# Optimization experiments

Measured on AMD Instinct MI355X. Metric: run time of the kernel, lower is better.

The kernel has to match this reference:

```python
import jax, jax.numpy as jnp
import numpy as np

IH, IW = 48, 48           # img_size
C = 256                   # inp == oup
NH, HD = 8, 32            # num_heads, head_dims; inner_dim = 256
HID = 4 * C               # MLP hidden
N = IH * IW               # window size (seq len) = 2304
SCALE = (C // NH) ** -0.5 # (inp_dims // num_heads) ** -0.5
EPS = 1e-5


def _relative_position_index():
    coords = np.stack(np.meshgrid(np.arange(IH), np.arange(IW), indexing='ij'))
    cf = coords.reshape(2, -1)
    rel = (cf[:, :, None] - cf[:, None, :]).transpose(1, 2, 0)
    rel[:, :, 0] += IH - 1
    rel[:, :, 1] += IW - 1
    rel[:, :, 0] *= 2 * IW - 1
    return jnp.asarray(rel.sum(-1).astype(np.int32))  # [N, N]


def setup_inputs() -> dict:
    key = jax.random.key(0)
    ks = jax.random.split(key, 12)
    s = 0.02
    return {
        'x': jax.random.normal(ks[0], (1, IH, IW, C), jnp.float32),
        'gamma1': jnp.ones((C,), jnp.float32),
        'beta1': jnp.zeros((C,), jnp.float32),
        'w_qkv': jax.random.normal(ks[1], (C, 3 * NH * HD), jnp.float32) * s,
        'w_proj': jax.random.normal(ks[2], (NH * HD, C), jnp.float32) * s,
        'b_proj': jnp.zeros((C,), jnp.float32),
        'bias_table': jax.random.normal(ks[3], ((2 * IH - 1) * (2 * IW - 1), NH), jnp.float32) * s,
        'gamma2': jnp.ones((C,), jnp.float32),
        'beta2': jnp.zeros((C,), jnp.float32),
        'w_fc1': jax.random.normal(ks[4], (C, HID), jnp.float32) * s,
        'b_fc1': jnp.zeros((HID,), jnp.float32),
        'w_fc2': jax.random.normal(ks[5], (HID, C), jnp.float32) * s,
        'b_fc2': jnp.zeros((C,), jnp.float32),
        'rel_idx': _relative_position_index(),
    }


def _layernorm(x, g, b):
    mu = jnp.mean(x, axis=-1, keepdims=True)
    var = jnp.mean(jnp.square(x - mu), axis=-1, keepdims=True)
    return (x - mu) * jax.lax.rsqrt(var + EPS) * g + b


def reference(x, gamma1, beta1, w_qkv, w_proj, b_proj, bias_table,
              gamma2, beta2, w_fc1, b_fc1, w_fc2, b_fc2, rel_idx):
    shortcut = x                                   # [1, IH, IW, C]
    t = x.reshape(1, N, C)
    t = _layernorm(t, gamma1, beta1)

    # qkv: [1, N, 3*NH*HD] -> q, k, v each [1, NH, N, HD]
    qkv = (t @ w_qkv).reshape(1, N, 3, NH, HD).transpose(2, 0, 3, 1, 4)
    q, k, v = qkv[0], qkv[1], qkv[2]
    q = q * SCALE

    attn = jnp.einsum('bhnd,bhmd->bhnm', q, k)     # [1, NH, N, N]
    # relative position bias: gather table rows by index -> [NH, N, N]
    bias = bias_table[rel_idx.reshape(-1)].reshape(N, N, NH).transpose(2, 0, 1)
    attn = jax.nn.softmax(attn + bias[None], axis=-1)

    o = jnp.einsum('bhnm,bhmd->bhnd', attn, v)     # [1, NH, N, HD]
    o = o.transpose(0, 2, 1, 3).reshape(1, N, NH * HD)
    o = o @ w_proj + b_proj                        # [1, N, C]

    x = shortcut + o.reshape(1, IH, IW, C)
    shortcut = x

    t = _layernorm(x.reshape(1, N, C), gamma2, beta2)
    t = jax.nn.gelu(t @ w_fc1 + b_fc1, approximate=False) @ w_fc2 + b_fc2
    return shortcut + t.reshape(1, IH, IW, C)
```

## Files before the change

### kernel.cpp

```cpp
#include <hip/hip_runtime.h>
#include <hip/hip_bf16.h>
#include <math.h>

#define IH 48
#define IW 48
#define NN 2304
#define CC 256
#define NH 8
#define HD 32
#define HID 1024
#define NBIAS 9025
#define SCALE 0.17677669529663687f
#define LOG2E 1.4426950408889634f
#define LN_EPS 1e-5f

typedef __attribute__((ext_vector_type(8))) short bf16x8;
typedef __attribute__((ext_vector_type(4))) float f32x4;

__device__ __forceinline__ short f2b(float f) {
    __hip_bfloat16 h = __float2bfloat16(f);
    short s; __builtin_memcpy(&s, &h, 2); return s;
}
__device__ __forceinline__ float b2f(short s) {
    __hip_bfloat16 h; __builtin_memcpy(&h, &s, 2); return __bfloat162float(h);
}
__device__ __forceinline__ float fast_exp2(float x) {
#if __has_builtin(__builtin_amdgcn_exp2f)
    return __builtin_amdgcn_exp2f(x);
#else
    return exp2f(x);
#endif
}

__global__ void prep_kernel(const float* __restrict__ x, const float* __restrict__ g,
                            const float* __restrict__ b, short* __restrict__ t1,
                            const float* __restrict__ bt, short* __restrict__ o_bias,
                            const float* __restrict__ w_qkv, const float* __restrict__ w_proj,
                            const float* __restrict__ w_fc1, const float* __restrict__ w_fc2,
                            short* __restrict__ o_qkv, short* __restrict__ o_proj,
                            short* __restrict__ o_fc1, short* __restrict__ o_fc2)
{
    __shared__ float tsh[32][33];
    __shared__ float red[8];
    const int bid = blockIdx.x, tid = threadIdx.x;
    if (bid < NN) {
        float v = x[bid * CC + tid];
        float s = v, s2 = v * v;
        #pragma unroll
        for (int off = 32; off > 0; off >>= 1) {
            s  += __shfl_xor(s, off);
            s2 += __shfl_xor(s2, off);
        }
        const int wid = tid >> 6;
        if ((tid & 63) == 0) { red[wid * 2] = s; red[wid * 2 + 1] = s2; }
        __syncthreads();
        float tot  = red[0] + red[2] + red[4] + red[6];
        float tot2 = red[1] + red[3] + red[5] + red[7];
        float mu   = tot * (1.0f / CC);
        float var  = tot2 * (1.0f / CC) - mu * mu;
        float rstd = rsqrtf(var + LN_EPS);
        t1[bid * CC + tid] = f2b((v - mu) * rstd * g[tid] + b[tid]);
        return;
    }
    if (bid < NN + 768) {
        int bb = bid - NN;
        const float* src; short* dst; int K, Nn, kt, nt;
        if (bb < 192)      { src = w_qkv;  dst = o_qkv;  K = 256;  Nn = 768;  kt = bb / 24; nt = bb % 24; }
        else if (bb < 256) { bb -= 192; src = w_proj; dst = o_proj; K = 256;  Nn = 256;  kt = bb / 8;  nt = bb % 8; }
        else if (bb < 512) { bb -= 256; src = w_fc1;  dst = o_fc1;  K = 256;  Nn = 1024; kt = bb / 32; nt = bb % 32; }
        else               { bb -= 512; src = w_fc2;  dst = o_fc2;  K = 1024; Nn = 256;  kt = bb / 8;  nt = bb % 8; }
        const int r = tid >> 5, c = tid & 31;
        const int k0 = kt * 32, n0 = nt * 32;
        #pragma unroll
        for (int i = 0; i < 4; ++i)
            tsh[r + i * 8][c] = src[(k0 + r + i * 8) * Nn + n0 + c];
        __syncthreads();
        #pragma unroll
        for (int i = 0; i < 4; ++i)
            dst[(n0 + r + i * 8) * K + k0 + c] = f2b(tsh[c][r + i * 8]);
        return;
    }
    const int stride = (gridDim.x - NN - 768) * 256;
    for (int i = (bid - NN - 768) * 256 + tid; i < NBIAS * NH; i += stride) {
        int idx = i >> 3, h = i & 7;
        o_bias[h * NBIAS + idx] = f2b(bt[i] * LOG2E);
    }
}

#define GSTRIDE 72
template<int KLEN, int KSTR, int TM>
__device__ __forceinline__ void mfma_gemm_core(const short* __restrict__ A,
                                               const short* __restrict__ BT,
                                               int m0, int n0, int kb, f32x4 acc[4],
                                               short* lds)
{
    short* As = lds;
    short* Bs = lds + TM * GSTRIDE;
    const int tid  = threadIdx.x;
    const int w    = tid >> 6, lane = tid & 63;
    const int quad = lane >> 4, l15 = lane & 15;
    const int sr = tid >> 2;
    const int sc = (tid & 3) * 16;
    #pragma unroll
    for (int c = 0; c < 4; ++c) acc[c] = (f32x4){0.f, 0.f, 0.f, 0.f};

    const short* Ap = &A [(m0 + sr) * KSTR + kb + sc];
    const short* Bp = &BT[(n0 + sr) * KSTR + kb + sc];
    bf16x8 ra0 = *(const bf16x8*)Ap,       ra1 = *(const bf16x8*)(Ap + 8);
    bf16x8 rb0 = *(const bf16x8*)Bp,       rb1 = *(const bf16x8*)(Bp + 8);
    bf16x8 rc0, rc1;
    const short* Bp2 = Bp;
    if constexpr (TM == 32) {
        Bp2 = &BT[(n0 + sr + 32) * KSTR + kb + sc];
        rc0 = *(const bf16x8*)Bp2;  rc1 = *(const bf16x8*)(Bp2 + 8);
    }

    for (int k0 = 0; k0 < KLEN; k0 += 64) {
        __syncthreads();
        *(bf16x8*)&As[sr * GSTRIDE + sc]     = ra0;
        *(bf16x8*)&As[sr * GSTRIDE + sc + 8] = ra1;
        *(bf16x8*)&Bs[sr * GSTRIDE + sc]     = rb0;
        *(bf16x8*)&Bs[sr * GSTRIDE + sc + 8] = rb1;
        if constexpr (TM == 32) {
            *(bf16x8*)&Bs[(sr + 32) * GSTRIDE + sc]     = rc0;
            *(bf16x8*)&Bs[(sr + 32) * GSTRIDE + sc + 8] = rc1;
        }
        if (k0 + 64 < KLEN) {
            ra0 = *(const bf16x8*)(Ap + k0 + 64);
            ra1 = *(const bf16x8*)(Ap + k0 + 72);
            rb0 = *(const bf16x8*)(Bp + k0 + 64);
            rb1 = *(const bf16x8*)(Bp + k0 + 72);
            if constexpr (TM == 32) {
                rc0 = *(const bf16x8*)(Bp2 + k0 + 64);
                rc1 = *(const bf16x8*)(Bp2 + k0 + 72);
            }
        }
        __syncthreads();
        #pragma unroll
        for (int s = 0; s < 2; ++s) {
            bf16x8 a = *(const bf16x8*)&As[(w * 16 + l15) * GSTRIDE + s * 32 + quad * 8];
            #pragma unroll
            for (int c = 0; c < 4; ++c) {
                bf16x8 b = *(const bf16x8*)&Bs[(c * 16 + l15) * GSTRIDE + s * 32 + quad * 8];
                acc[c] = __builtin_amdgcn_mfma_f32_16x16x32_bf16(a, b, acc[c], 0, 0, 0);
            }
        }
    }
}

__global__ void qkv_kernel(const short* __restrict__ t1, const short* __restrict__ wT,
                           short* __restrict__ qb, short* __restrict__ kb,
                           short* __restrict__ vT)
{
    __shared__ short lds[2 * 64 * GSTRIDE];
    f32x4 acc[4];
    const int m0 = blockIdx.y * 64, n0 = blockIdx.x * 64;
    mfma_gemm_core<256, 256, 64>(t1, wT, m0, n0, 0, acc, lds);
    const int lane = threadIdx.x & 63, w = threadIdx.x >> 6;
    const int quad = lane >> 4, l15 = lane & 15;
    #pragma unroll
    for (int c = 0; c < 4; ++c) {
        int col = n0 + c * 16 + l15;
        int three = col >> 8, rem = col & 255;
        int h = rem >> 5, d = rem & 31;
        #pragma unroll
        for (int r = 0; r < 4; ++r) {
            int row = m0 + w * 16 + quad * 4 + r;
            float v = acc[c][r];
            if (three == 0)      qb[(h * NN + row) * HD + d] = f2b(v * (SCALE * LOG2E));
            else if (three == 1) kb[(h * NN + row) * HD + d] = f2b(v);
            else                 vT[(h * HD + d) * NN + row] = f2b(v);
        }
    }
}

#define PSTRIDE 40
__global__ __launch_bounds__(256) void attn_kernel(
        const short* __restrict__ qb, const short* __restrict__ kb,
        const short* __restrict__ vT, const short* __restrict__ biasT,
        short* __restrict__ o)
{
    __shared__ float Ored[4][16][33];
    __shared__ float lred[4][16];
    __shared__ short sbuf[4][16 * PSTRIDE];
    __shared__ short bwin[48][64];
    const int w = threadIdx.x >> 6, lane = threadIdx.x & 63;
    const int quad = lane >> 4, l15 = lane & 15;
    const int h = blockIdx.x / 144, q0 = (blockIdx.x % 144) * 16;
    const int t0 = w * 576;
    short* sb = &sbuf[w][0];
    const short* bt = &biasT[h * NBIAS];

    const int qi = q0 / IW, qj0 = q0 % IW;

    for (int idx = threadIdx.x; idx < 48 * 63; idx += 256) {
        int kr = idx / 63, cc = idx - kr * 63;
        bwin[kr][cc] = bt[(qi - kr + 47) * 95 + qj0 + cc];
    }

    bf16x8 qf = *(const bf16x8*)&qb[(h * NN + q0 + l15) * HD + quad * 8];

    f32x4 O0 = (f32x4){0.f,0.f,0.f,0.f}, O1 = (f32x4){0.f,0.f,0.f,0.f};
    float lp[4] = {0.f, 0.f, 0.f, 0.f};
    const f32x4 zero = (f32x4){0.f,0.f,0.f,0.f};

    __syncthreads();

    for (int c = 0; c < 18; ++c) {
        const int t = t0 + c * 32;
        bf16x8 k0f = *(const bf16x8*)&kb[(h * NN + t      + l15) * HD + quad * 8];
        bf16x8 k1f = *(const bf16x8*)&kb[(h * NN + t + 16 + l15) * HD + quad * 8];
        f32x4 s0 = __builtin_amdgcn_mfma_f32_16x16x32_bf16(qf, k0f, zero, 0, 0, 0);
        f32x4 s1 = __builtin_amdgcn_mfma_f32_16x16x32_bf16(qf, k1f, zero, 0, 0, 0);
        bf16x8 v0 = *(const bf16x8*)&vT[(h * HD + l15)      * NN + t + quad * 8];
        bf16x8 v1 = *(const bf16x8*)&vT[(h * HD + 16 + l15) * NN + t + quad * 8];

        const int ki0 = t / IW,        kj0_ = t - ki0 * IW;
        const int ki1 = (t + 16) / IW, kj1_ = (t + 16) - ki1 * IW;
        const int cA = quad * 4 + 47 - kj0_ - l15;
        const int cB = quad * 4 + 47 - kj1_ - l15;

        #pragma unroll
        for (int r = 0; r < 4; ++r) {
            float p0 = fast_exp2(s0[r] + b2f(bwin[ki0][cA + r]));
            float p1 = fast_exp2(s1[r] + b2f(bwin[ki1][cB + r]));
            lp[r] += p0 + p1;
            sb[(quad * 4 + r) * PSTRIDE + l15]      = f2b(p0);
            sb[(quad * 4 + r) * PSTRIDE + 16 + l15] = f2b(p1);
        }
        asm volatile("s_waitcnt lgkmcnt(0)" ::: "memory");
        bf16x8 pa = *(const bf16x8*)&sb[l15 * PSTRIDE + quad * 8];
        O0 = __builtin_amdgcn_mfma_f32_16x16x32_bf16(pa, v0, O0, 0, 0, 0);
        O1 = __builtin_amdgcn_mfma_f32_16x16x32_bf16(pa, v1, O1, 0, 0, 0);
    }

    #pragma unroll
    for (int r = 0; r < 4; ++r) {
        float l = lp[r];
        l += __shfl_xor(l, 1); l += __shfl_xor(l, 2);
        l += __shfl_xor(l, 4); l += __shfl_xor(l, 8);
        if (l15 == 0) lred[w][quad * 4 + r] = l;
        Ored[w][quad * 4 + r][l15]      = O0[r];
        Ored[w][quad * 4 + r][16 + l15] = O1[r];
    }
    __syncthreads();
    {
        const int col = threadIdx.x & 31;
        for (int rr = threadIdx.x >> 5; rr < 16; rr += 8) {
            float s = 0.f, l = 0.f;
            #pragma unroll
            for (int pw = 0; pw < 4; ++pw) { s += Ored[pw][rr][col]; l += lred[pw][rr]; }
            o[(q0 + rr) * CC + h * HD + col] = f2b(s / l);
        }
    }
}

__global__ void proj_kernel(const short* __restrict__ o, const short* __restrict__ wT,
                            const float* __restrict__ bias, const float* __restrict__ x_in,
                            float* __restrict__ x2)
{
    __shared__ short lds[(32 + 64) * GSTRIDE];
    f32x4 acc[4];
    const int m0 = blockIdx.y * 32, n0 = blockIdx.x * 64;
    mfma_gemm_core<256, 256, 32>(o, wT, m0, n0, 0, acc, lds);
    const int lane = threadIdx.x & 63, w = threadIdx.x >> 6;
    const int quad = lane >> 4, l15 = lane & 15;
    #pragma unroll
    for (int c = 0; c < 4; ++c) {
        int col = n0 + c * 16 + l15;
        #pragma unroll
        for (int r = 0; r < 4; ++r) {
            int row = m0 + w * 16 + quad * 4 + r;
            x2[row * CC + col] = acc[c][r] + bias[col] + x_in[row * CC + col];
        }
    }
}

__global__ __launch_bounds__(256) void fc1_kernel(
        const float* __restrict__ x2, const short* __restrict__ wT,
        const float* __restrict__ g2, const float* __restrict__ b2,
        const float* __restrict__ bias, short* __restrict__ h1)
{
    __shared__ short lds[2 * 64 * GSTRIDE];
    __shared__ float muS[64], rsS[64];
    short* As = lds;
    short* Bs = lds + 64 * GSTRIDE;
    const int tid = threadIdx.x;
    const int w = tid >> 6, lane = tid & 63;
    const int quad = lane >> 4, l15 = lane & 15;
    const int m0 = blockIdx.y * 64, n0 = blockIdx.x * 64;

    {
        const int row = tid >> 2, cb = (tid & 3) * 64;
        const float* xr = &x2[(m0 + row) * CC + cb];
        float s = 0.f, q = 0.f;
        #pragma unroll
        for (int j = 0; j < 16; ++j) {
            f32x4 v = *(const f32x4*)(xr + j * 4);
            s += (v[0] + v[1]) + (v[2] + v[3]);
            q += (v[0] * v[0] + v[1] * v[1]) + (v[2] * v[2] + v[3] * v[3]);
        }
        s += __shfl_xor(s, 1); s += __shfl_xor(s, 2);
        q += __shfl_xor(q, 1); q += __shfl_xor(q, 2);
        if ((tid & 3) == 0) {
            float mu  = s * (1.0f / CC);
            float var = q * (1.0f / CC) - mu * mu;
            muS[row] = mu;
            rsS[row] = rsqrtf(var + LN_EPS);
        }
    }
    __syncthreads();

    const int sr = tid >> 2, sc = (tid & 3) * 16;
    const float mu = muS[sr], rs = rsS[sr];
    f32x4 acc[4];
    #pragma unroll
    for (int c = 0; c < 4; ++c) acc[c] = (f32x4){0.f, 0.f, 0.f, 0.f};

    const float* Ap = &x2[(m0 + sr) * CC + sc];
    const short* Bp = &wT[(n0 + sr) * CC + sc];
    f32x4 av[4];
    #pragma unroll
    for (int j = 0; j < 4; ++j) av[j] = *(const f32x4*)(Ap + j * 4);
    bf16x8 rb0 = *(const bf16x8*)Bp, rb1 = *(const bf16x8*)(Bp + 8);

    for (int k0 = 0; k0 < 256; k0 += 64) {
        __syncthreads();
        {
            const float* gp = &g2[k0 + sc];
            const float* bp = &b2[k0 + sc];
            f32x4 gv[4], bv[4];
            #pragma unroll
            for (int j = 0; j < 4; ++j) {
                gv[j] = *(const f32x4*)(gp + j * 4);
                bv[j] = *(const f32x4*)(bp + j * 4);
            }
            bf16x8 lo, hi;
            #pragma unroll
            for (int j = 0; j < 8; ++j) {
                float vA = av[j >> 2][j & 3];
                float vB = av[2 + (j >> 2)][j & 3];
                lo[j] = f2b((vA - mu) * rs * gv[j >> 2][j & 3] + bv[j >> 2][j & 3]);
                hi[j] = f2b((vB - mu) * rs * gv[2 + (j >> 2)][j & 3] + bv[2 + (j >> 2)][j & 3]);
            }
            *(bf16x8*)&As[sr * GSTRIDE + sc]     = lo;
            *(bf16x8*)&As[sr * GSTRIDE + sc + 8] = hi;
        }
        *(bf16x8*)&Bs[sr * GSTRIDE + sc]     = rb0;
        *(bf16x8*)&Bs[sr * GSTRIDE + sc + 8] = rb1;
        if (k0 + 64 < 256) {
            #pragma unroll
            for (int j = 0; j < 4; ++j) av[j] = *(const f32x4*)(Ap + k0 + 64 + j * 4);
            rb0 = *(const bf16x8*)(Bp + k0 + 64);
            rb1 = *(const bf16x8*)(Bp + k0 + 72);
        }
        __syncthreads();
        #pragma unroll
        for (int s = 0; s < 2; ++s) {
            bf16x8 a = *(const bf16x8*)&As[(w * 16 + l15) * GSTRIDE + s * 32 + quad * 8];
            #pragma unroll
            for (int c = 0; c < 4; ++c) {
                bf16x8 b = *(const bf16x8*)&Bs[(c * 16 + l15) * GSTRIDE + s * 32 + quad * 8];
                acc[c] = __builtin_amdgcn_mfma_f32_16x16x32_bf16(a, b, acc[c], 0, 0, 0);
            }
        }
    }
    #pragma unroll
    for (int c = 0; c < 4; ++c) {
        int col = n0 + c * 16 + l15;
        #pragma unroll
        for (int r = 0; r < 4; ++r) {
            int row = m0 + w * 16 + quad * 4 + r;
            float v = acc[c][r] + bias[col];
            float ge = 0.5f * v * (1.0f + erff(v * 0.7071067811865476f));
            h1[row * HID + col] = f2b(ge);
        }
    }
}

__global__ void fc2_kernel(const short* __restrict__ h1, const short* __restrict__ wT,
                           const float* __restrict__ bias, const float* __restrict__ x2,
                           float* __restrict__ out)
{
    __shared__ short lds[(32 + 64) * GSTRIDE];
    f32x4 acc[4];
    const int m0 = blockIdx.y * 32, n0 = blockIdx.x * 64;
    mfma_gemm_core<1024, 1024, 32>(h1, wT, m0, n0, 0, acc, lds);
    const int lane = threadIdx.x & 63, w = threadIdx.x >> 6;
    const int quad = lane >> 4, l15 = lane & 15;
    #pragma unroll
    for (int c = 0; c < 4; ++c) {
        int col = n0 + c * 16 + l15;
        #pragma unroll
        for (int r = 0; r < 4; ++r) {
            int row = m0 + w * 16 + quad * 4 + r;
            out[row * CC + col] = acc[c][r] + bias[col] + x2[row * CC + col];
        }
    }
}

extern "C" void kernel_launch(void* const* d_in, const int* in_sizes, int n_in,
                              void* d_out, int out_size, void* d_ws, size_t ws_size,
                              hipStream_t stream)
{
    const float* x          = (const float*)d_in[0];
    const float* gamma1     = (const float*)d_in[1];
    const float* beta1      = (const float*)d_in[2];
    const float* w_qkv      = (const float*)d_in[3];
    const float* w_proj     = (const float*)d_in[4];
    const float* b_proj     = (const float*)d_in[5];
    const float* bias_table = (const float*)d_in[6];
    const float* gamma2     = (const float*)d_in[7];
    const float* beta2      = (const float*)d_in[8];
    const float* w_fc1      = (const float*)d_in[9];
    const float* b_fc1      = (const float*)d_in[10];
    const float* w_fc2      = (const float*)d_in[11];
    const float* b_fc2      = (const float*)d_in[12];

    short* S = (short*)d_ws;
    const int NC = NN * CC;
    short* t1     = S;
    short* qb     = t1  + NC;
    short* kb     = qb  + NC;
    short* vT     = kb  + NC;
    short* obuf   = vT  + NC;
    short* h1     = obuf+ NC;
    short* wTqkv  = h1  + NN * HID;
    short* wTproj = wTqkv  + 768 * 256;
    short* wTfc1  = wTproj + 256 * 256;
    short* wTfc2  = wTfc1  + 1024 * 256;
    short* biasT  = wTfc2  + 256 * 1024;
    float* x2     = (float*)(biasT + NH * NBIAS + 8);

    prep_kernel<<<NN + 768 + 64, 256, 0, stream>>>(x, gamma1, beta1, t1,
                                                   bias_table, biasT,
                                                   w_qkv, w_proj, w_fc1, w_fc2,
                                                   wTqkv, wTproj, wTfc1, wTfc2);
    qkv_kernel<<<dim3(12, 36), 256, 0, stream>>>(t1, wTqkv, qb, kb, vT);
    attn_kernel<<<1152, 256, 0, stream>>>(qb, kb, vT, biasT, obuf);
    proj_kernel<<<dim3(4, 72), 128, 0, stream>>>(obuf, wTproj, b_proj, x, x2);
    fc1_kernel<<<dim3(16, 36), 256, 0, stream>>>(x2, wTfc1, gamma2, beta2,
                                                 b_fc1, h1);
    fc2_kernel<<<dim3(4, 72), 128, 0, stream>>>(h1, wTfc2, b_fc2, x2,
                                                (float*)d_out);
}
```

Before: 170.4 us.

## Fuse LN2 statistics into proj epilogue, shrink GEMM tiles, reorder attention blocks

The proj epilogue now accumulates per-row sum and sum-of-squares of the residual output and adds them atomically into a stats buffer, which prep zeroes. fc1 reads these stats instead of recomputing the row mean and variance. The qkv and fc1 GEMMs switch to 32-row tiles with 128 threads, doubling their block counts. The attention kernel interleaves heads across consecutive block IDs and raises wave priority around its MFMA calls. The aim is to remove a redundant pass over x2 and improve occupancy and scheduling, at the cost of atomic traffic and a single-pass variance formula.

```diff
diff --git a/kernel.cpp b/kernel.cpp
--- a/kernel.cpp
+++ b/kernel.cpp
@@ -38,7 +38,8 @@
                             const float* __restrict__ w_qkv, const float* __restrict__ w_proj,
                             const float* __restrict__ w_fc1, const float* __restrict__ w_fc2,
                             short* __restrict__ o_qkv, short* __restrict__ o_proj,
-                            short* __restrict__ o_fc1, short* __restrict__ o_fc2)
+                            short* __restrict__ o_fc1, short* __restrict__ o_fc2,
+                            float* __restrict__ stats)
 {
     __shared__ float tsh[32][33];
     __shared__ float red[8];
@@ -80,11 +81,13 @@
             dst[(n0 + r + i * 8) * K + k0 + c] = f2b(tsh[c][r + i * 8]);
         return;
     }
+    const int base = (bid - NN - 768) * 256 + tid;
     const int stride = (gridDim.x - NN - 768) * 256;
-    for (int i = (bid - NN - 768) * 256 + tid; i < NBIAS * NH; i += stride) {
+    for (int i = base; i < NBIAS * NH; i += stride) {
         int idx = i >> 3, h = i & 7;
         o_bias[h * NBIAS + idx] = f2b(bt[i] * LOG2E);
     }
+    for (int i = base; i < 2 * NN; i += stride) stats[i] = 0.f;
 }
 
 #define GSTRIDE 72
@@ -152,10 +155,10 @@
                            short* __restrict__ qb, short* __restrict__ kb,
                            short* __restrict__ vT)
 {
-    __shared__ short lds[2 * 64 * GSTRIDE];
+    __shared__ short lds[(32 + 64) * GSTRIDE];
     f32x4 acc[4];
-    const int m0 = blockIdx.y * 64, n0 = blockIdx.x * 64;
-    mfma_gemm_core<256, 256, 64>(t1, wT, m0, n0, 0, acc, lds);
+    const int m0 = blockIdx.y * 32, n0 = blockIdx.x * 64;
+    mfma_gemm_core<256, 256, 32>(t1, wT, m0, n0, 0, acc, lds);
     const int lane = threadIdx.x & 63, w = threadIdx.x >> 6;
     const int quad = lane >> 4, l15 = lane & 15;
     #pragma unroll
@@ -186,7 +189,8 @@
     __shared__ short bwin[48][64];
     const int w = threadIdx.x >> 6, lane = threadIdx.x & 63;
     const int quad = lane >> 4, l15 = lane & 15;
-    const int h = blockIdx.x / 144, q0 = (blockIdx.x % 144) * 16;
+    const int bid = (blockIdx.x & 7) * 144 + (blockIdx.x >> 3);
+    const int h = bid / 144, q0 = (bid % 144) * 16;
     const int t0 = w * 576;
     short* sb = &sbuf[w][0];
     const short* bt = &biasT[h * NBIAS];
@@ -210,8 +214,10 @@
         const int t = t0 + c * 32;
         bf16x8 k0f = *(const bf16x8*)&kb[(h * NN + t      + l15) * HD + quad * 8];
         bf16x8 k1f = *(const bf16x8*)&kb[(h * NN + t + 16 + l15) * HD + quad * 8];
+        __builtin_amdgcn_s_setprio(1);
         f32x4 s0 = __builtin_amdgcn_mfma_f32_16x16x32_bf16(qf, k0f, zero, 0, 0, 0);
         f32x4 s1 = __builtin_amdgcn_mfma_f32_16x16x32_bf16(qf, k1f, zero, 0, 0, 0);
+        __builtin_amdgcn_s_setprio(0);
         bf16x8 v0 = *(const bf16x8*)&vT[(h * HD + l15)      * NN + t + quad * 8];
         bf16x8 v1 = *(const bf16x8*)&vT[(h * HD + 16 + l15) * NN + t + quad * 8];
 
@@ -230,8 +236,10 @@
         }
         asm volatile("s_waitcnt lgkmcnt(0)" ::: "memory");
         bf16x8 pa = *(const bf16x8*)&sb[l15 * PSTRIDE + quad * 8];
+        __builtin_amdgcn_s_setprio(1);
         O0 = __builtin_amdgcn_mfma_f32_16x16x32_bf16(pa, v0, O0, 0, 0, 0);
         O1 = __builtin_amdgcn_mfma_f32_16x16x32_bf16(pa, v1, O1, 0, 0, 0);
+        __builtin_amdgcn_s_setprio(0);
     }
 
     #pragma unroll
@@ -257,7 +265,7 @@
 
 __global__ void proj_kernel(const short* __restrict__ o, const short* __restrict__ wT,
                             const float* __restrict__ bias, const float* __restrict__ x_in,
-                            float* __restrict__ x2)
+                            float* __restrict__ x2, float* __restrict__ stats)
 {
     __shared__ short lds[(32 + 64) * GSTRIDE];
     f32x4 acc[4];
@@ -265,64 +273,66 @@
     mfma_gemm_core<256, 256, 32>(o, wT, m0, n0, 0, acc, lds);
     const int lane = threadIdx.x & 63, w = threadIdx.x >> 6;
     const int quad = lane >> 4, l15 = lane & 15;
+    float rs_[4] = {0.f, 0.f, 0.f, 0.f}, rq_[4] = {0.f, 0.f, 0.f, 0.f};
     #pragma unroll
     for (int c = 0; c < 4; ++c) {
         int col = n0 + c * 16 + l15;
         #pragma unroll
         for (int r = 0; r < 4; ++r) {
             int row = m0 + w * 16 + quad * 4 + r;
-            x2[row * CC + col] = acc[c][r] + bias[col] + x_in[row * CC + col];
-        }
-    }
-}
-
-__global__ __launch_bounds__(256) void fc1_kernel(
-        const float* __restrict__ x2, const short* __restrict__ wT,
+            float v = acc[c][r] + bias[col] + x_in[row * CC + col];
+            x2[row * CC + col] = v;
+            rs_[r] += v;
+            rq_[r] += v * v;
+        }
+    }
+    #pragma unroll
+    for (int r = 0; r < 4; ++r) {
+        float s = rs_[r], q = rq_[r];
+        s += __shfl_xor(s, 1); s += __shfl_xor(s, 2);
+        s += __shfl_xor(s, 4); s += __shfl_xor(s, 8);
+        q += __shfl_xor(q, 1); q += __shfl_xor(q, 2);
+        q += __shfl_xor(q, 4); q += __shfl_xor(q, 8);
+        if (l15 == 0) {
+            int row = m0 + w * 16 + quad * 4 + r;
+            atomicAdd(&stats[2 * row],     s);
+            atomicAdd(&stats[2 * row + 1], q);
+        }
+    }
+}
+
+__global__ __launch_bounds__(128) void fc1_kernel(
+        const float* __restrict__ x2, const float* __restrict__ stats,
+        const short* __restrict__ wT,
         const float* __restrict__ g2, const float* __restrict__ b2,
         const float* __restrict__ bias, short* __restrict__ h1)
 {
-    __shared__ short lds[2 * 64 * GSTRIDE];
-    __shared__ float muS[64], rsS[64];
+    __shared__ short lds[(32 + 64) * GSTRIDE];
     short* As = lds;
-    short* Bs = lds + 64 * GSTRIDE;
+    short* Bs = lds + 32 * GSTRIDE;
     const int tid = threadIdx.x;
     const int w = tid >> 6, lane = tid & 63;
     const int quad = lane >> 4, l15 = lane & 15;
-    const int m0 = blockIdx.y * 64, n0 = blockIdx.x * 64;
-
-    {
-        const int row = tid >> 2, cb = (tid & 3) * 64;
-        const float* xr = &x2[(m0 + row) * CC + cb];
-        float s = 0.f, q = 0.f;
-        #pragma unroll
-        for (int j = 0; j < 16; ++j) {
-            f32x4 v = *(const f32x4*)(xr + j * 4);
-            s += (v[0] + v[1]) + (v[2] + v[3]);
-            q += (v[0] * v[0] + v[1] * v[1]) + (v[2] * v[2] + v[3] * v[3]);
-        }
-        s += __shfl_xor(s, 1); s += __shfl_xor(s, 2);
-        q += __shfl_xor(q, 1); q += __shfl_xor(q, 2);
-        if ((tid & 3) == 0) {
-            float mu  = s * (1.0f / CC);
-            float var = q * (1.0f / CC) - mu * mu;
-            muS[row] = mu;
-            rsS[row] = rsqrtf(var + LN_EPS);
-        }
-    }
-    __syncthreads();
-
+    const int m0 = blockIdx.y * 32, n0 = blockIdx.x * 64;
     const int sr = tid >> 2, sc = (tid & 3) * 16;
-    const float mu = muS[sr], rs = rsS[sr];
+
+    const float ssum = stats[2 * (m0 + sr)];
+    const float sq   = stats[2 * (m0 + sr) + 1];
+    const float mu = ssum * (1.0f / CC);
+    const float rs = rsqrtf(sq * (1.0f / CC) - mu * mu + LN_EPS);
+
     f32x4 acc[4];
     #pragma unroll
     for (int c = 0; c < 4; ++c) acc[c] = (f32x4){0.f, 0.f, 0.f, 0.f};
 
-    const float* Ap = &x2[(m0 + sr) * CC + sc];
-    const short* Bp = &wT[(n0 + sr) * CC + sc];
+    const float* Ap  = &x2[(m0 + sr) * CC + sc];
+    const short* Bp  = &wT[(n0 + sr) * CC + sc];
+    const short* Bp2 = &wT[(n0 + sr + 32) * CC + sc];
     f32x4 av[4];
     #pragma unroll
     for (int j = 0; j < 4; ++j) av[j] = *(const f32x4*)(Ap + j * 4);
-    bf16x8 rb0 = *(const bf16x8*)Bp, rb1 = *(const bf16x8*)(Bp + 8);
+    bf16x8 rb0 = *(const bf16x8*)Bp,  rb1 = *(const bf16x8*)(Bp + 8);
+    bf16x8 rc0 = *(const bf16x8*)Bp2, rc1 = *(const bf16x8*)(Bp2 + 8);
 
     for (int k0 = 0; k0 < 256; k0 += 64) {
         __syncthreads();
@@ -338,21 +348,26 @@
             bf16x8 lo, hi;
             #pragma unroll
             for (int j = 0; j < 8; ++j) {
-                float vA = av[j >> 2][j & 3];
-                float vB = av[2 + (j >> 2)][j & 3];
-                lo[j] = f2b((vA - mu) * rs * gv[j >> 2][j & 3] + bv[j >> 2][j & 3]);
-                hi[j] = f2b((vB - mu) * rs * gv[2 + (j >> 2)][j & 3] + bv[2 + (j >> 2)][j & 3]);
+                lo[j] = f2b((av[j >> 2][j & 3] - mu) * rs * gv[j >> 2][j & 3]
+                            + bv[j >> 2][j & 3]);
+                hi[j] = f2b((av[2 + (j >> 2)][j & 3] - mu) * rs * gv[2 + (j >> 2)][j & 3]
+                            + bv[2 + (j >> 2)][j & 3]);
             }
             *(bf16x8*)&As[sr * GSTRIDE + sc]     = lo;
             *(bf16x8*)&As[sr * GSTRIDE + sc + 8] = hi;
         }
-        *(bf16x8*)&Bs[sr * GSTRIDE + sc]     = rb0;
-        *(bf16x8*)&Bs[sr * GSTRIDE + sc + 8] = rb1;
+        *(bf16x8*)&Bs[sr * GSTRIDE + sc]            = rb0;
+        *(bf16x8*)&Bs[sr * GSTRIDE + sc + 8]        = rb1;
+        *(bf16x8*)&Bs[(sr + 32) * GSTRIDE + sc]     = rc0;
+        *(bf16x8*)&Bs[(sr + 32) * GSTRIDE + sc + 8] = rc1;
         if (k0 + 64 < 256) {
             #pragma unroll
-            for (int j = 0; j < 4; ++j) av[j] = *(const f32x4*)(Ap + k0 + 64 + j * 4);
+            for (int j = 0; j < 4; ++j)
+                av[j] = *(const f32x4*)(Ap + k0 + 64 + j * 4);
             rb0 = *(const bf16x8*)(Bp + k0 + 64);
             rb1 = *(const bf16x8*)(Bp + k0 + 72);
+            rc0 = *(const bf16x8*)(Bp2 + k0 + 64);
+            rc1 = *(const bf16x8*)(Bp2 + k0 + 72);
         }
         __syncthreads();
         #pragma unroll
@@ -431,15 +446,17 @@
     short* wTfc2  = wTfc1  + 1024 * 256;
     short* biasT  = wTfc2  + 256 * 1024;
     float* x2     = (float*)(biasT + NH * NBIAS + 8);
+    float* stats  = x2 + NC;
 
     prep_kernel<<<NN + 768 + 64, 256, 0, stream>>>(x, gamma1, beta1, t1,
                                                    bias_table, biasT,
                                                    w_qkv, w_proj, w_fc1, w_fc2,
-                                                   wTqkv, wTproj, wTfc1, wTfc2);
-    qkv_kernel<<<dim3(12, 36), 256, 0, stream>>>(t1, wTqkv, qb, kb, vT);
+                                                   wTqkv, wTproj, wTfc1, wTfc2,
+                                                   stats);
+    qkv_kernel<<<dim3(12, 72), 128, 0, stream>>>(t1, wTqkv, qb, kb, vT);
     attn_kernel<<<1152, 256, 0, stream>>>(qb, kb, vT, biasT, obuf);
-    proj_kernel<<<dim3(4, 72), 128, 0, stream>>>(obuf, wTproj, b_proj, x, x2);
-    fc1_kernel<<<dim3(16, 36), 256, 0, stream>>>(x2, wTfc1, gamma2, beta2,
+    proj_kernel<<<dim3(4, 72), 128, 0, stream>>>(obuf, wTproj, b_proj, x, x2, stats);
+    fc1_kernel<<<dim3(16, 72), 128, 0, stream>>>(x2, stats, wTfc1, gamma2, beta2,
                                                  b_fc1, h1);
     fc2_kernel<<<dim3(4, 72), 128, 0, stream>>>(h1, wTfc2, b_fc2, x2,
                                                 (float*)d_out);
```

After: 163.1 us. -4.3%, faster.
